# Optimization experiments

Measured on AMD Instinct MI355X. Metric: run time of the kernel, lower is better.

The kernel has to match this reference:

```python
import jax, jax.numpy as jnp
import numpy as np

N = 50000      # nodes
E = 800000     # edges (before self-loops)
IN = 256       # in_channels
H = 4          # heads (layer 1)
C = 64         # hidden per head
OUT = 40       # out_channels / classes


def setup_inputs() -> dict:
    key = jax.random.key(0)
    ks = jax.random.split(key, 10)
    s = 0.05  # weight init scale
    return {
        "x": jax.random.normal(ks[0], (N, IN), jnp.float32),
        "edge_index": jax.random.randint(ks[1], (2, E), 0, N),
        "W1": jax.random.normal(ks[2], (IN, H * C), jnp.float32) * s,
        "a_src1": jax.random.normal(ks[3], (H, C), jnp.float32) * s,
        "a_dst1": jax.random.normal(ks[4], (H, C), jnp.float32) * s,
        "b1": jnp.zeros((H * C,), jnp.float32),
        "W2": jax.random.normal(ks[5], (H * C, OUT), jnp.float32) * s,
        "a_src2": jax.random.normal(ks[6], (1, OUT), jnp.float32) * s,
        "a_dst2": jax.random.normal(ks[7], (1, OUT), jnp.float32) * s,
        "b2": jnp.zeros((OUT,), jnp.float32),
    }


def _gat_layer(x, src, dst, W, a_src, a_dst, bias, heads, out_c):
    """PyG GATConv (concat=True, negative_slope=0.2, self-loops already in src/dst)."""
    n = x.shape[0]
    h = (x @ W).reshape(n, heads, out_c)                    # [N,H,C]
    al_s = jnp.sum(h * a_src, axis=-1)                      # [N,H]
    al_d = jnp.sum(h * a_dst, axis=-1)                      # [N,H]
    e = jax.nn.leaky_relu(al_s[src] + al_d[dst], 0.2)       # [Etot,H]
    # edge softmax over incoming edges of each destination node
    m = jax.ops.segment_max(e, dst, num_segments=n)         # [N,H]
    ee = jnp.exp(e - m[dst])
    denom = jax.ops.segment_sum(ee, dst, num_segments=n)
    alpha = ee / (denom[dst] + 1e-16)                       # [Etot,H]
    msg = alpha[:, :, None] * h[src]                        # [Etot,H,C]
    out = jax.ops.segment_sum(msg, dst, num_segments=n)     # [N,H,C]
    return out.reshape(n, heads * out_c) + bias


def reference(x, edge_index, W1, a_src1, a_dst1, b1, W2, a_src2, a_dst2, b2):
    n = x.shape[0]
    loops = jnp.arange(n, dtype=edge_index.dtype)
    src = jnp.concatenate([edge_index[0], loops])
    dst = jnp.concatenate([edge_index[1], loops])
    h = _gat_layer(x, src, dst, W1, a_src1, a_dst1, b1, H, C)   # [N, H*C]
    h = jax.nn.relu(h)
    # F.dropout in eval mode is identity (reference run in eval mode)
    out = _gat_layer(h, src, dst, W2, a_src2, a_dst2, b2, 1, OUT)  # [N, OUT]
    return jax.nn.log_softmax(out, axis=1)
```

## Files before the change

### kernel.cpp

```cpp
#include <hip/hip_runtime.h>
#include <hip/hip_bf16.h>

typedef __hip_bfloat16 bf16;
typedef short v8s __attribute__((ext_vector_type(8)));
typedef float v4f __attribute__((ext_vector_type(4)));

constexpr int NN    = 50000;
constexpr int NE    = 800000;
constexpr int CIN   = 256;
constexpr int HC    = 256;
constexpr int NH    = 4;
constexpr int NOUT  = 40;
constexpr int NPAD  = 48;
constexpr int SCB   = 196;
constexpr int B1    = 128;
constexpr int CH    = (NE + B1 - 1) / B1;
constexpr int NB    = (NN + 255) >> 8;

constexpr size_t al256(size_t x){ return (x + 255) & ~(size_t)255; }
constexpr size_t WS_FLAGS = 0;
constexpr size_t WS_EW1   = 256;
constexpr size_t WS_W1T   = al256(WS_EW1   + (size_t)NE*16);
constexpr size_t WS_AS1N  = al256(WS_W1T   + (size_t)CIN*HC*2);
constexpr size_t WS_AD1N  = al256(WS_AS1N  + HC*2);
constexpr size_t WS_B1N   = al256(WS_AD1N  + HC*2);
constexpr size_t WS_W2T   = al256(WS_B1N   + HC*2);
constexpr size_t WS_AS2N  = al256(WS_W2T   + (size_t)NPAD*HC*2);
constexpr size_t WS_AD2N  = al256(WS_AS2N  + NOUT*2);
constexpr size_t WS_B2N   = al256(WS_AD2N  + NOUT*2);
constexpr size_t WS_COUNTS= al256(WS_B2N   + NOUT*2);
constexpr size_t WS_CURSOR= al256(WS_COUNTS+ (size_t)NN*4);
constexpr size_t WS_ROWPTR= al256(WS_CURSOR+ (size_t)NN*4);
constexpr size_t WS_EIDX  = al256(WS_ROWPTR+ (size_t)(NN+1)*4);
constexpr size_t WS_H1    = al256(WS_EIDX  + (size_t)NE*4);
constexpr size_t WS_ALS1  = al256(WS_H1    + (size_t)NN*HC);
constexpr size_t WS_ALD1  = al256(WS_ALS1  + (size_t)NN*NH*4);
constexpr size_t WS_Y1    = al256(WS_ALD1  + (size_t)NN*NH*4);
constexpr size_t WS_H2    = al256(WS_Y1    + (size_t)NN*HC*2);
constexpr size_t WS_ALS2  = al256(WS_H2    + (size_t)NN*NOUT*2);
constexpr size_t WS_ALD2  = al256(WS_ALS2  + (size_t)NN*4);
constexpr size_t WS_EW2   = al256(WS_ALD2  + (size_t)NN*4);
constexpr size_t WS_BSUM  = al256(WS_EW2   + (size_t)NE*4);
constexpr size_t WS_BOFF  = al256(WS_BSUM  + 1024);
constexpr size_t WS_GCNT  = al256(WS_BOFF  + 1024);
constexpr size_t WS_ROFF  = al256(WS_GCNT  + (size_t)256*B1*4);
constexpr size_t WS_BBASE = al256(WS_ROFF  + (size_t)256*B1*4);
constexpr size_t WS_EBUF  = al256(WS_BBASE + 1056);

constexpr int CV_W1  = 0;
constexpr int CV_AS1 = CV_W1  + CIN*HC;
constexpr int CV_AD1 = CV_AS1 + HC;
constexpr int CV_B1  = CV_AD1 + HC;
constexpr int CV_W2  = CV_B1  + HC;
constexpr int CV_AS2 = CV_W2  + HC*NOUT;
constexpr int CV_AD2 = CV_AS2 + NOUT;
constexpr int CV_B2  = CV_AD2 + NOUT;
constexpr int CV_HIST= CV_B2  + NOUT;
constexpr int CV_END = CV_HIST + NE;

__device__ __forceinline__ float b2f(bf16 v) { return __bfloat162float(v); }
__device__ __forceinline__ bf16  f2b(float v){ return __float2bfloat16(v); }
__device__ __forceinline__ float bits2f(unsigned short u){ return __uint_as_float(((unsigned)u) << 16); }
__device__ __forceinline__ unsigned short f2bits(float v){
  bf16 t = __float2bfloat16(v);
  return *reinterpret_cast<unsigned short*>(&t);
}
__device__ __forceinline__ float lrelu(float x){ return x > 0.f ? x : 0.2f * x; }

__device__ __forceinline__ float wave_sum(float v){
  #pragma unroll
  for (int off = 32; off; off >>= 1) v += __shfl_xor(v, off, 64);
  return v;
}
__device__ __forceinline__ float wave_max(float v){
  #pragma unroll
  for (int off = 32; off; off >>= 1) v = fmaxf(v, __shfl_xor(v, off, 64));
  return v;
}

__global__ __launch_bounds__(64) void k_detect(const unsigned short* __restrict__ xu,
                                               const unsigned* __restrict__ eu,
                                               int* __restrict__ flags){
  int lane = threadIdx.x;
  int cnt = 0;
  for (int i = lane; i < 256; i += 64){
    int e = (xu[i] >> 7) & 0xFF;
    cnt += (e >= 0x60 && e <= 0x8F) ? 1 : 0;
  }
  #pragma unroll
  for (int off = 32; off; off >>= 1) cnt += __shfl_xor(cnt, off, 64);
  unsigned odd = eu[2 * lane + 1];
  #pragma unroll
  for (int off = 32; off; off >>= 1) odd |= __shfl_xor(odd, off, 64);
  if (lane == 0){
    flags[0] = (cnt < 218) ? 1 : 0;
    flags[1] = (odd == 0)  ? 1 : 0;
  }
}

__device__ __forceinline__ bf16 cvt_b(const void* src, int i, int f32m){
  if (f32m) return __float2bfloat16(((const float*)src)[i]);
  return ((const bf16*)src)[i];
}

__global__ __launch_bounds__(256) void k_convert(
    const void* __restrict__ W1,
    const void* __restrict__ as1,const void* __restrict__ ad1,
    const void* __restrict__ b1, const void* __restrict__ W2,
    const void* __restrict__ as2,const void* __restrict__ ad2,
    const void* __restrict__ b2, const void* __restrict__ ei,
    char* __restrict__ ws){
  const int* flags = (const int*)(ws + WS_FLAGS);
  int f32m = flags[0], i64m = flags[1];
  bf16* w1t  = (bf16*)(ws + WS_W1T);
  bf16* as1n = (bf16*)(ws + WS_AS1N);
  bf16* ad1n = (bf16*)(ws + WS_AD1N);
  bf16* b1n  = (bf16*)(ws + WS_B1N);
  bf16* w2t  = (bf16*)(ws + WS_W2T);
  bf16* as2n = (bf16*)(ws + WS_AS2N);
  bf16* ad2n = (bf16*)(ws + WS_AD2N);
  bf16* b2n  = (bf16*)(ws + WS_B2N);
  int*  counts=(int*) (ws + WS_COUNTS);
  for (int g = blockIdx.x * 256 + threadIdx.x; g < CV_END; g += gridDim.x * 256){
    if      (g < CV_AS1){ int i = g-CV_W1; int k = i >> 8, n = i & 255;
      w1t[n*CIN + k] = cvt_b(W1, i, f32m); }
    else if (g < CV_AD1) as1n[g-CV_AS1] = cvt_b(as1,g-CV_AS1, f32m);
    else if (g < CV_B1 ) ad1n[g-CV_AD1] = cvt_b(ad1,g-CV_AD1, f32m);
    else if (g < CV_W2 ) b1n [g-CV_B1 ] = cvt_b(b1, g-CV_B1,  f32m);
    else if (g < CV_AS2){ int i = g-CV_W2; int k = i / NOUT, n = i - k*NOUT;
      w2t[n*CIN + k] = cvt_b(W2, i, f32m); }
    else if (g < CV_AD2) as2n[g-CV_AS2] = cvt_b(as2,g-CV_AS2, f32m);
    else if (g < CV_B2 ) ad2n[g-CV_AD2] = cvt_b(ad2,g-CV_AD2, f32m);
    else if (g < CV_HIST) b2n[g-CV_B2 ] = cvt_b(b2, g-CV_B2,  f32m);
    else { int i = g-CV_HIST;
      int d = i64m ? (int)((const long long*)ei)[(size_t)NE+i] : ((const int*)ei)[NE+i];
      atomicAdd(&counts[d], 1); }
  }
}

__global__ __launch_bounds__(256) void k_scan_part(const int* __restrict__ counts, int* __restrict__ bsum){
  __shared__ int lds[256];
  int t = threadIdx.x;
  int idx = blockIdx.x * 256 + t;
  int v = (idx < NN) ? counts[idx] : 0;
  lds[t] = v;
  #pragma unroll
  for (int s = 128; s > 0; s >>= 1){
    __syncthreads();
    if (t < s) lds[t] += lds[t + s];
  }
  if (t == 0) bsum[blockIdx.x] = lds[0];
}

__global__ __launch_bounds__(256) void k_scan_mid(const int* __restrict__ bsum, int* __restrict__ boff,
                                                  int* __restrict__ row_ptr){
  __shared__ int lds[256];
  int t = threadIdx.x;
  int v = (t < SCB) ? bsum[t] : 0;
  lds[t] = v;
  for (int off = 1; off < 256; off <<= 1){
    __syncthreads();
    int u = (t >= off) ? lds[t - off] : 0;
    __syncthreads();
    lds[t] += u;
  }
  __syncthreads();
  if (t < SCB) boff[t] = lds[t] - v;
  if (t == 0) row_ptr[NN] = NE;
}

__global__ __launch_bounds__(256) void k_scan_apply(const int* __restrict__ counts, const int* __restrict__ boff,
                                                    int* __restrict__ row_ptr){
  __shared__ int lds[256];
  int t = threadIdx.x;
  int idx = blockIdx.x * 256 + t;
  int v = (idx < NN) ? counts[idx] : 0;
  lds[t] = v;
  for (int off = 1; off < 256; off <<= 1){
    __syncthreads();
    int u = (t >= off) ? lds[t - off] : 0;
    __syncthreads();
    lds[t] += u;
  }
  __syncthreads();
  if (idx < NN) row_ptr[idx] = boff[blockIdx.x] + lds[t] - v;
}

__global__ __launch_bounds__(256) void k_lhist(const void* __restrict__ ei, const int* __restrict__ flags,
                                               int* __restrict__ gcnt){
  __shared__ int h[256];
  int tid = threadIdx.x, blk = blockIdx.x;
  h[tid] = 0;
  __syncthreads();
  int i0 = blk * CH, i1 = min(i0 + CH, NE);
  int i64m = flags[1];
  for (int i = i0 + tid; i < i1; i += 256){
    int d = i64m ? (int)((const long long*)ei)[(size_t)NE + i] : ((const int*)ei)[NE + i];
    atomicAdd(&h[d >> 8], 1);
  }
  __syncthreads();
  gcnt[tid * B1 + blk] = h[tid];
}

__global__ __launch_bounds__(256) void k_gscan(const int* __restrict__ gcnt, int* __restrict__ roff,
                                               int* __restrict__ bbase){
  __shared__ int lds[256];
  int t = threadIdx.x;
  int tot = 0;
  for (int blk = 0; blk < B1; ++blk) tot += gcnt[t * B1 + blk];
  lds[t] = tot;
  for (int off = 1; off < 256; off <<= 1){
    __syncthreads();
    int u = (t >= off) ? lds[t - off] : 0;
    __syncthreads();
    lds[t] += u;
  }
  __syncthreads();
  int base = lds[t] - tot;
  bbase[t] = base;
  if (t == 255) bbase[256] = NE;
  int run = base;
  for (int blk = 0; blk < B1; ++blk){
    roff[t * B1 + blk] = run;
    run += gcnt[t * B1 + blk];
  }
}

__global__ __launch_bounds__(256) void k_bscatter(const void* __restrict__ ei, const int* __restrict__ flags,
                                                  const int* __restrict__ roff, int2* __restrict__ ebuf){
  __shared__ int lcur[256];
  int tid = threadIdx.x, blk = blockIdx.x;
  lcur[tid] = roff[tid * B1 + blk];
  __syncthreads();
  int i0 = blk * CH, i1 = min(i0 + CH, NE);
  int i64m = flags[1];
  for (int i = i0 + tid; i < i1; i += 256){
    int s, d;
    if (i64m){ s = (int)((const long long*)ei)[i]; d = (int)((const long long*)ei)[(size_t)NE + i]; }
    else     { s = ((const int*)ei)[i];            d = ((const int*)ei)[NE + i]; }
    int pos = atomicAdd(&lcur[d >> 8], 1);
    ebuf[pos] = make_int2(s, d);
  }
}

__global__ __launch_bounds__(256) void k_refine(const int2* __restrict__ ebuf, const int* __restrict__ bbase,
                                                const int* __restrict__ row_ptr, int* __restrict__ cursor,
                                                int* __restrict__ eidx){
  int b = blockIdx.x;
  int p0 = bbase[b], p1 = bbase[b + 1];
  for (int p = p0 + threadIdx.x; p < p1; p += 256){
    int2 e = ebuf[p];
    int pos = row_ptr[e.y] + atomicAdd(&cursor[e.y], 1);
    eidx[pos] = e.x;
  }
}

constexpr int G1R = 64;
constexpr int LP  = 72;
__global__ __launch_bounds__(256) void k_gemm1(const void* __restrict__ xin,
                                               const int* __restrict__ flags,
                                               const bf16* __restrict__ w1t,
                                               const bf16* __restrict__ as1, const bf16* __restrict__ ad1,
                                               unsigned char* __restrict__ h1q,
                                               float* __restrict__ al_s1, float* __restrict__ al_d1){
  __shared__ short Ab[G1R * LP];
  __shared__ short Bb[256 * LP];
  int tid  = threadIdx.x;
  int w    = tid >> 6, lane = tid & 63, quad = lane >> 4, c = lane & 15;
  int row0 = blockIdx.x * G1R;
  int f32m = flags[0];

  v4f acc[4][4];
  #pragma unroll
  for (int mt = 0; mt < 4; ++mt)
    #pragma unroll
    for (int nt = 0; nt < 4; ++nt) acc[mt][nt] = (v4f){0.f,0.f,0.f,0.f};

  int arow = tid >> 2;
  int aseg = tid & 3;
  int grow = row0 + arow; if (grow >= NN) grow = NN - 1;

  for (int ph = 0; ph < 4; ++ph){
    if (ph) __syncthreads();
    {
      short va[16];
      if (f32m){
        const float* src = (const float*)xin + (size_t)grow * CIN + ph*64 + aseg*16;
        #pragma unroll
        for (int i = 0; i < 4; ++i){
          float4 f = *reinterpret_cast<const float4*>(src + i*4);
          va[i*4+0] = (short)f2bits(f.x); va[i*4+1] = (short)f2bits(f.y);
          va[i*4+2] = (short)f2bits(f.z); va[i*4+3] = (short)f2bits(f.w);
        }
      } else {
        const short* src = (const short*)xin + (size_t)grow * CIN + ph*64 + aseg*16;
        v8s u0 = *reinterpret_cast<const v8s*>(src);
        v8s u1 = *reinterpret_cast<const v8s*>(src + 8);
        #pragma unroll
        for (int i = 0; i < 8; ++i){ va[i] = u0[i]; va[8+i] = u1[i]; }
      }
      short* dst = &Ab[arow * LP + aseg * 16];
      *reinterpret_cast<v8s*>(dst)     = *reinterpret_cast<v8s*>(&va[0]);
      *reinterpret_cast<v8s*>(dst + 8) = *reinterpret_cast<v8s*>(&va[8]);
    }
    {
      const short* src = (const short*)w1t + (size_t)tid * CIN + ph*64;
      short* dst = &Bb[tid * LP];
      #pragma unroll
      for (int j = 0; j < 8; ++j)
        *reinterpret_cast<v8s*>(dst + j*8) = *reinterpret_cast<const v8s*>(src + j*8);
    }
    __syncthreads();
    #pragma unroll
    for (int s = 0; s < 2; ++s){
      int ch = s*4 + quad;
      v8s af[4], bfb[4];
      #pragma unroll
      for (int mt = 0; mt < 4; ++mt)
        af[mt] = *reinterpret_cast<const v8s*>(&Ab[(mt*16 + c) * LP + ch*8]);
      #pragma unroll
      for (int nt = 0; nt < 4; ++nt)
        bfb[nt] = *reinterpret_cast<const v8s*>(&Bb[(w*64 + nt*16 + c) * LP + ch*8]);
      #pragma unroll
      for (int mt = 0; mt < 4; ++mt)
        #pragma unroll
        for (int nt = 0; nt < 4; ++nt)
          acc[mt][nt] = __builtin_amdgcn_mfma_f32_16x16x32_bf16(af[mt], bfb[nt], acc[mt][nt], 0, 0, 0);
    }
  }

  float as1v[4], ad1v[4];
  #pragma unroll
  for (int nt = 0; nt < 4; ++nt){
    as1v[nt] = b2f(as1[w*64 + nt*16 + c]);
    ad1v[nt] = b2f(ad1[w*64 + nt*16 + c]);
  }
  #pragma unroll
  for (int mt = 0; mt < 4; ++mt){
    #pragma unroll
    for (int r = 0; r < 4; ++r){
      float ps = 0.f, pd = 0.f;
      #pragma unroll
      for (int nt = 0; nt < 4; ++nt){ ps += acc[mt][nt][r] * as1v[nt]; pd += acc[mt][nt][r] * ad1v[nt]; }
      #pragma unroll
      for (int off = 1; off < 16; off <<= 1){ ps += __shfl_xor(ps, off, 64); pd += __shfl_xor(pd, off, 64); }
      int row = row0 + mt*16 + quad*4 + r;
      if (c == 0 && row < NN){
        al_s1[row * NH + w] = ps;
        al_d1[row * NH + w] = pd;
      }
    }
  }
  #pragma unroll
  for (int mt = 0; mt < 4; ++mt){
    #pragma unroll
    for (int nt = 0; nt < 4; ++nt){
      #pragma unroll
      for (int r = 0; r < 4; r += 2){
        int row = row0 + mt*16 + quad*4 + r;
        if (row + 1 < NN){
          int pk = __builtin_amdgcn_cvt_pk_fp8_f32(acc[mt][nt][r], acc[mt][nt][r+1], 0, false);
          size_t col = w*64 + nt*16 + c;
          h1q[(size_t)row       * HC + col] = (unsigned char)(pk & 0xFF);
          h1q[(size_t)(row + 1) * HC + col] = (unsigned char)((pk >> 8) & 0xFF);
        } else if (row < NN){
          int pk = __builtin_amdgcn_cvt_pk_fp8_f32(acc[mt][nt][r], acc[mt][nt][r], 0, false);
          h1q[(size_t)row * HC + w*64 + nt*16 + c] = (unsigned char)(pk & 0xFF);
        }
      }
    }
  }
}

__global__ __launch_bounds__(256) void k_ew1(const int* __restrict__ row_ptr, const int* __restrict__ eidx,
                                             const float* __restrict__ al_s1, const float* __restrict__ al_d1,
                                             float4* __restrict__ ew1){
  int lane = threadIdx.x & 63;
  int n = blockIdx.x * 4 + (threadIdx.x >> 6);
  int p0 = __builtin_amdgcn_readfirstlane(row_ptr[n]);
  int p1 = __builtin_amdgcn_readfirstlane(row_ptr[n + 1]);
  float4 ad = reinterpret_cast<const float4*>(al_d1)[n];
  for (int p = p0 + lane; p < p1; p += 64){
    int s = eidx[p];
    float4 as = reinterpret_cast<const float4*>(al_s1)[s];
    float4 w;
    w.x = __expf(lrelu(as.x + ad.x));
    w.y = __expf(lrelu(as.y + ad.y));
    w.z = __expf(lrelu(as.z + ad.z));
    w.w = __expf(lrelu(as.w + ad.w));
    ew1[p] = w;
  }
}

__global__ __launch_bounds__(256) void k_gather1(const int* __restrict__ row_ptr, const int* __restrict__ eidx,
                                                 const float* __restrict__ ew1,
                                                 const float* __restrict__ al_s1, const float* __restrict__ al_d1,
                                                 const unsigned* __restrict__ h1v, const bf16* __restrict__ b1,
                                                 bf16* __restrict__ y1){
  int lane = threadIdx.x & 63;
  int n = blockIdx.x * 4 + (threadIdx.x >> 6);
  int h = lane >> 4;
  int p0 = __builtin_amdgcn_readfirstlane(row_ptr[n]);
  int p1 = __builtin_amdgcn_readfirstlane(row_ptr[n + 1]);
  float wss = __expf(lrelu(al_s1[n * NH + h] + al_d1[n * NH + h]));
  unsigned us = h1v[(size_t)n * 64 + lane];
  float den = wss;
  float a0 = wss * __builtin_amdgcn_cvt_f32_fp8(us, 0);
  float a1 = wss * __builtin_amdgcn_cvt_f32_fp8(us, 1);
  float a2 = wss * __builtin_amdgcn_cvt_f32_fp8(us, 2);
  float a3 = wss * __builtin_amdgcn_cvt_f32_fp8(us, 3);
  int p = p0;
  for (; p + 1 < p1; p += 2){
    int sA = __builtin_amdgcn_readfirstlane(eidx[p]);
    int sB = __builtin_amdgcn_readfirstlane(eidx[p + 1]);
    float wA = ew1[(size_t)p * 4 + h];
    float wB = ew1[(size_t)(p + 1) * 4 + h];
    unsigned uA = h1v[(size_t)sA * 64 + lane];
    unsigned uB = h1v[(size_t)sB * 64 + lane];
    den += wA + wB;
    a0 += wA * __builtin_amdgcn_cvt_f32_fp8(uA, 0) + wB * __builtin_amdgcn_cvt_f32_fp8(uB, 0);
    a1 += wA * __builtin_amdgcn_cvt_f32_fp8(uA, 1) + wB * __builtin_amdgcn_cvt_f32_fp8(uB, 1);
    a2 += wA * __builtin_amdgcn_cvt_f32_fp8(uA, 2) + wB * __builtin_amdgcn_cvt_f32_fp8(uB, 2);
    a3 += wA * __builtin_amdgcn_cvt_f32_fp8(uA, 3) + wB * __builtin_amdgcn_cvt_f32_fp8(uB, 3);
  }
  if (p < p1){
    int s = __builtin_amdgcn_readfirstlane(eidx[p]);
    float w = ew1[(size_t)p * 4 + h];
    unsigned u = h1v[(size_t)s * 64 + lane];
    den += w;
    a0 += w * __builtin_amdgcn_cvt_f32_fp8(u, 0);
    a1 += w * __builtin_amdgcn_cvt_f32_fp8(u, 1);
    a2 += w * __builtin_amdgcn_cvt_f32_fp8(u, 2);
    a3 += w * __builtin_amdgcn_cvt_f32_fp8(u, 3);
  }
  float inv = 1.f / (den + 1e-16f);
  ushort4 bb = reinterpret_cast<const ushort4*>(b1)[lane];
  ushort4 o;
  o.x = f2bits(fmaxf(a0 * inv + bits2f(bb.x), 0.f));
  o.y = f2bits(fmaxf(a1 * inv + bits2f(bb.y), 0.f));
  o.z = f2bits(fmaxf(a2 * inv + bits2f(bb.z), 0.f));
  o.w = f2bits(fmaxf(a3 * inv + bits2f(bb.w), 0.f));
  reinterpret_cast<ushort4*>(y1)[(size_t)n * 64 + lane] = o;
}

constexpr int W2LP = 260;
__global__ __launch_bounds__(256) void k_gemm2(const bf16* __restrict__ y1, const bf16* __restrict__ w2t,
                                               const bf16* __restrict__ as2, const bf16* __restrict__ ad2,
                                               bf16* __restrict__ h2, float* __restrict__ al_s2,
                                               float* __restrict__ al_d2){
  __shared__ short Wb[NPAD * W2LP];
  int tid = threadIdx.x;
  int w = tid >> 6, lane = tid & 63, quad = lane >> 4, c = lane & 15;
  int m0 = blockIdx.x * 64 + w * 16;
  for (int idx = tid; idx < NPAD * 32; idx += 256){
    int n = idx >> 5, sg = idx & 31;
    *reinterpret_cast<v8s*>(&Wb[n * W2LP + sg * 8]) =
      *reinterpret_cast<const v8s*>((const short*)w2t + (size_t)n * CIN + sg * 8);
  }
  int arow = m0 + c; if (arow >= NN) arow = NN - 1;
  const short* ar = (const short*)y1 + (size_t)arow * HC + quad * 8;
  v8s a[8];
  #pragma unroll
  for (int i = 0; i < 8; ++i) a[i] = *reinterpret_cast<const v8s*>(ar + i * 32);
  __syncthreads();

  v4f acc[3];
  #pragma unroll
  for (int t = 0; t < 3; ++t) acc[t] = (v4f){0.f, 0.f, 0.f, 0.f};
  #pragma unroll
  for (int k = 0; k < 8; ++k){
    int ch = k*4 + quad;
    #pragma unroll
    for (int t = 0; t < 3; ++t){
      v8s b = *reinterpret_cast<const v8s*>(&Wb[(t*16 + c) * W2LP + ch * 8]);
      acc[t] = __builtin_amdgcn_mfma_f32_16x16x32_bf16(a[k], b, acc[t], 0, 0, 0);
    }
  }
  float as2f[3], ad2f[3];
  #pragma unroll
  for (int t = 0; t < 3; ++t){
    int col = t*16 + c;
    as2f[t] = (col < NOUT) ? b2f(as2[col]) : 0.f;
    ad2f[t] = (col < NOUT) ? b2f(ad2[col]) : 0.f;
  }
  #pragma unroll
  for (int r = 0; r < 4; ++r){
    int row = m0 + quad*4 + r;
    float ps = 0.f, pd = 0.f;
    #pragma unroll
    for (int t = 0; t < 3; ++t){ ps += acc[t][r] * as2f[t]; pd += acc[t][r] * ad2f[t]; }
    #pragma unroll
    for (int off = 1; off < 16; off <<= 1){ ps += __shfl_xor(ps, off, 64); pd += __shfl_xor(pd, off, 64); }
    if (row < NN){
      if (c == 0){ al_s2[row] = ps; al_d2[row] = pd; }
      #pragma unroll
      for (int t = 0; t < 3; ++t){
        int col = t*16 + c;
        if (col < NOUT) h2[(size_t)row * NOUT + col] = f2b(acc[t][r]);
      }
    }
  }
}

__global__ __launch_bounds__(256) void k_ew2(const int* __restrict__ row_ptr, const int* __restrict__ eidx,
                                             const float* __restrict__ al_s2, const float* __restrict__ al_d2,
                                             float* __restrict__ ew2){
  int lane = threadIdx.x & 63;
  int n = blockIdx.x * 4 + (threadIdx.x >> 6);
  int p0 = __builtin_amdgcn_readfirstlane(row_ptr[n]);
  int p1 = __builtin_amdgcn_readfirstlane(row_ptr[n + 1]);
  float ad = al_d2[n];
  for (int p = p0 + lane; p < p1; p += 64)
    ew2[p] = __expf(lrelu(al_s2[eidx[p]] + ad));
}

__global__ __launch_bounds__(256) void k_gather2(const int* __restrict__ row_ptr, const int* __restrict__ eidx,
                                                 const float* __restrict__ ew2,
                                                 const float* __restrict__ al_s2, const float* __restrict__ al_d2,
                                                 const bf16* __restrict__ h2, const bf16* __restrict__ b2v,
                                                 const int* __restrict__ flags, void* __restrict__ out){
  int lane = threadIdx.x & 63;
  int n = blockIdx.x * 4 + (threadIdx.x >> 6);
  int p0 = __builtin_amdgcn_readfirstlane(row_ptr[n]);
  int p1 = __builtin_amdgcn_readfirstlane(row_ptr[n + 1]);
  float wss = __expf(lrelu(al_s2[n] + al_d2[n]));
  float den = wss;
  float acc = (lane < NOUT) ? wss * b2f(h2[(size_t)n * NOUT + lane]) : 0.f;
  int p = p0;
  for (; p + 1 < p1; p += 2){
    int sA = __builtin_amdgcn_readfirstlane(eidx[p]);
    int sB = __builtin_amdgcn_readfirstlane(eidx[p + 1]);
    float wA = ew2[p], wB = ew2[p + 1];
    float hA = 0.f, hB = 0.f;
    if (lane < NOUT){
      hA = b2f(h2[(size_t)sA * NOUT + lane]);
      hB = b2f(h2[(size_t)sB * NOUT + lane]);
    }
    den += wA + wB;
    acc += wA * hA + wB * hB;
  }
  if (p < p1){
    int s = __builtin_amdgcn_readfirstlane(eidx[p]);
    float w = ew2[p];
    den += w;
    if (lane < NOUT) acc += w * b2f(h2[(size_t)s * NOUT + lane]);
  }
  float v = (lane < NOUT) ? (acc / (den + 1e-16f) + b2f(b2v[lane])) : -INFINITY;
  float M = wave_max(v);
  float ex = (lane < NOUT) ? __expf(v - M) : 0.f;
  float S = wave_sum(ex);
  if (lane < NOUT){
    float r = v - M - __logf(S);
    size_t idx = (size_t)n * NOUT + lane;
    if (flags[0]) ((float*)out)[idx] = r;
    else          ((bf16*)out)[idx]  = f2b(r);
  }
}

extern "C" void kernel_launch(void* const* d_in, const int* in_sizes, int n_in,
                              void* d_out, int out_size, void* d_ws, size_t ws_size,
                              hipStream_t stream) {
  const void* x   = d_in[0];
  const void* ei  = d_in[1];
  const void* W1  = d_in[2];
  const void* as1 = d_in[3];
  const void* ad1 = d_in[4];
  const void* b1  = d_in[5];
  const void* W2  = d_in[6];
  const void* as2 = d_in[7];
  const void* ad2 = d_in[8];
  const void* b2  = d_in[9];

  char* ws = (char*)d_ws;
  int*   flags   = (int*)  (ws + WS_FLAGS);
  float* ew1     = (float*)(ws + WS_EW1);
  bf16*  w1t     = (bf16*) (ws + WS_W1T);
  bf16*  as1n    = (bf16*) (ws + WS_AS1N);
  bf16*  ad1n    = (bf16*) (ws + WS_AD1N);
  bf16*  b1n     = (bf16*) (ws + WS_B1N);
  bf16*  w2t     = (bf16*) (ws + WS_W2T);
  bf16*  as2n    = (bf16*) (ws + WS_AS2N);
  bf16*  ad2n    = (bf16*) (ws + WS_AD2N);
  bf16*  b2n     = (bf16*) (ws + WS_B2N);
  int*   counts  = (int*)  (ws + WS_COUNTS);
  int*   cursor  = (int*)  (ws + WS_CURSOR);
  int*   row_ptr = (int*)  (ws + WS_ROWPTR);
  int*   eidx    = (int*)  (ws + WS_EIDX);
  unsigned char* h1q = (unsigned char*)(ws + WS_H1);
  float* al_s1   = (float*)(ws + WS_ALS1);
  float* al_d1   = (float*)(ws + WS_ALD1);
  bf16*  y1      = (bf16*) (ws + WS_Y1);
  bf16*  h2      = (bf16*) (ws + WS_H2);
  float* al_s2   = (float*)(ws + WS_ALS2);
  float* al_d2   = (float*)(ws + WS_ALD2);
  float* ew2     = (float*)(ws + WS_EW2);
  int*   bsum    = (int*)  (ws + WS_BSUM);
  int*   boff    = (int*)  (ws + WS_BOFF);
  int*   gcnt    = (int*)  (ws + WS_GCNT);
  int*   roff    = (int*)  (ws + WS_ROFF);
  int*   bbase   = (int*)  (ws + WS_BBASE);
  int2*  ebuf    = (int2*) (ws + WS_EBUF);

  hipMemsetAsync(counts, 0, (size_t)NN * 4, stream);
  hipMemsetAsync(cursor, 0, (size_t)NN * 4, stream);
  hipMemsetAsync(w2t,    0, (size_t)NPAD * CIN * 2, stream);

  k_detect <<<1, 64, 0, stream>>>((const unsigned short*)x, (const unsigned*)ei, flags);
  k_convert<<<1024, 256, 0, stream>>>(W1, as1, ad1, b1, W2, as2, ad2, b2, ei, ws);

  k_lhist   <<<B1, 256, 0, stream>>>(ei, flags, gcnt);
  k_gscan   <<<1, 256, 0, stream>>>(gcnt, roff, bbase);
  k_scan_part <<<SCB, 256, 0, stream>>>(counts, bsum);
  k_scan_mid  <<<1, 256, 0, stream>>>(bsum, boff, row_ptr);
  k_scan_apply<<<SCB, 256, 0, stream>>>(counts, boff, row_ptr);
  k_bscatter<<<B1, 256, 0, stream>>>(ei, flags, roff, ebuf);
  k_refine  <<<NB, 256, 0, stream>>>(ebuf, bbase, row_ptr, cursor, eidx);

  k_gemm1  <<<(NN + G1R - 1) / G1R, 256, 0, stream>>>(x, flags, w1t, as1n, ad1n, h1q, al_s1, al_d1);
  k_ew1    <<<NN / 4, 256, 0, stream>>>(row_ptr, eidx, al_s1, al_d1, (float4*)ew1);
  k_gather1<<<NN / 4, 256, 0, stream>>>(row_ptr, eidx, ew1, al_s1, al_d1, (const unsigned*)h1q, b1n, y1);
  k_gemm2  <<<(NN + 63) / 64, 256, 0, stream>>>(y1, w2t, as2n, ad2n, h2, al_s2, al_d2);
  k_ew2    <<<NN / 4, 256, 0, stream>>>(row_ptr, eidx, al_s2, al_d2, ew2);
  k_gather2<<<NN / 4, 256, 0, stream>>>(row_ptr, eidx, ew2, al_s2, al_d2, h2, b2n, flags, d_out);
}
```

Baseline: 347.3 us.

## Store layer-2 features as FP8 and split gather2 edges across quarter-waves

Layer-2 projected features are now written by gemm2 as FP8 bytes in a 64-byte row stride instead of bf16 rows of 40. gather2 splits each node's edge list across four 16-lane groups, each handling every fourth edge. Each lane unpacks four FP8 channels, and the partial sums are then combined with cross-lane shuffles. Gather1's inner loop is also unrolled from 2 to 4 edges to expose more outstanding loads. The goal is less gather traffic and more memory-level parallelism, at the cost of extra FP8 quantization error on layer-2 activations and byte-granular scattered writes in gemm2.

```diff
diff --git a/kernel.cpp b/kernel.cpp
--- a/kernel.cpp
+++ b/kernel.cpp
@@ -37,7 +37,7 @@
 constexpr size_t WS_ALD1  = al256(WS_ALS1  + (size_t)NN*NH*4);
 constexpr size_t WS_Y1    = al256(WS_ALD1  + (size_t)NN*NH*4);
 constexpr size_t WS_H2    = al256(WS_Y1    + (size_t)NN*HC*2);
-constexpr size_t WS_ALS2  = al256(WS_H2    + (size_t)NN*NOUT*2);
+constexpr size_t WS_ALS2  = al256(WS_H2    + (size_t)NN*64);
 constexpr size_t WS_ALD2  = al256(WS_ALS2  + (size_t)NN*4);
 constexpr size_t WS_EW2   = al256(WS_ALD2  + (size_t)NN*4);
 constexpr size_t WS_BSUM  = al256(WS_EW2   + (size_t)NE*4);
@@ -410,20 +410,30 @@
   float a2 = wss * __builtin_amdgcn_cvt_f32_fp8(us, 2);
   float a3 = wss * __builtin_amdgcn_cvt_f32_fp8(us, 3);
   int p = p0;
-  for (; p + 1 < p1; p += 2){
+  for (; p + 3 < p1; p += 4){
     int sA = __builtin_amdgcn_readfirstlane(eidx[p]);
     int sB = __builtin_amdgcn_readfirstlane(eidx[p + 1]);
+    int sC = __builtin_amdgcn_readfirstlane(eidx[p + 2]);
+    int sD = __builtin_amdgcn_readfirstlane(eidx[p + 3]);
     float wA = ew1[(size_t)p * 4 + h];
     float wB = ew1[(size_t)(p + 1) * 4 + h];
+    float wC = ew1[(size_t)(p + 2) * 4 + h];
+    float wD = ew1[(size_t)(p + 3) * 4 + h];
     unsigned uA = h1v[(size_t)sA * 64 + lane];
     unsigned uB = h1v[(size_t)sB * 64 + lane];
-    den += wA + wB;
-    a0 += wA * __builtin_amdgcn_cvt_f32_fp8(uA, 0) + wB * __builtin_amdgcn_cvt_f32_fp8(uB, 0);
-    a1 += wA * __builtin_amdgcn_cvt_f32_fp8(uA, 1) + wB * __builtin_amdgcn_cvt_f32_fp8(uB, 1);
-    a2 += wA * __builtin_amdgcn_cvt_f32_fp8(uA, 2) + wB * __builtin_amdgcn_cvt_f32_fp8(uB, 2);
-    a3 += wA * __builtin_amdgcn_cvt_f32_fp8(uA, 3) + wB * __builtin_amdgcn_cvt_f32_fp8(uB, 3);
-  }
-  if (p < p1){
+    unsigned uC = h1v[(size_t)sC * 64 + lane];
+    unsigned uD = h1v[(size_t)sD * 64 + lane];
+    den += (wA + wB) + (wC + wD);
+    a0 += wA * __builtin_amdgcn_cvt_f32_fp8(uA, 0) + wB * __builtin_amdgcn_cvt_f32_fp8(uB, 0)
+        + wC * __builtin_amdgcn_cvt_f32_fp8(uC, 0) + wD * __builtin_amdgcn_cvt_f32_fp8(uD, 0);
+    a1 += wA * __builtin_amdgcn_cvt_f32_fp8(uA, 1) + wB * __builtin_amdgcn_cvt_f32_fp8(uB, 1)
+        + wC * __builtin_amdgcn_cvt_f32_fp8(uC, 1) + wD * __builtin_amdgcn_cvt_f32_fp8(uD, 1);
+    a2 += wA * __builtin_amdgcn_cvt_f32_fp8(uA, 2) + wB * __builtin_amdgcn_cvt_f32_fp8(uB, 2)
+        + wC * __builtin_amdgcn_cvt_f32_fp8(uC, 2) + wD * __builtin_amdgcn_cvt_f32_fp8(uD, 2);
+    a3 += wA * __builtin_amdgcn_cvt_f32_fp8(uA, 3) + wB * __builtin_amdgcn_cvt_f32_fp8(uB, 3)
+        + wC * __builtin_amdgcn_cvt_f32_fp8(uC, 3) + wD * __builtin_amdgcn_cvt_f32_fp8(uD, 3);
+  }
+  for (; p < p1; ++p){
     int s = __builtin_amdgcn_readfirstlane(eidx[p]);
     float w = ew1[(size_t)p * 4 + h];
     unsigned u = h1v[(size_t)s * 64 + lane];
@@ -446,7 +456,7 @@
 constexpr int W2LP = 260;
 __global__ __launch_bounds__(256) void k_gemm2(const bf16* __restrict__ y1, const bf16* __restrict__ w2t,
                                                const bf16* __restrict__ as2, const bf16* __restrict__ ad2,
-                                               bf16* __restrict__ h2, float* __restrict__ al_s2,
+                                               unsigned char* __restrict__ h2q, float* __restrict__ al_s2,
                                                float* __restrict__ al_d2){
   __shared__ short Wb[NPAD * W2LP];
   int tid = threadIdx.x;
@@ -491,12 +501,18 @@
     for (int t = 0; t < 3; ++t){ ps += acc[t][r] * as2f[t]; pd += acc[t][r] * ad2f[t]; }
     #pragma unroll
     for (int off = 1; off < 16; off <<= 1){ ps += __shfl_xor(ps, off, 64); pd += __shfl_xor(pd, off, 64); }
-    if (row < NN){
-      if (c == 0){ al_s2[row] = ps; al_d2[row] = pd; }
-      #pragma unroll
-      for (int t = 0; t < 3; ++t){
-        int col = t*16 + c;
-        if (col < NOUT) h2[(size_t)row * NOUT + col] = f2b(acc[t][r]);
+    if (row < NN && c == 0){ al_s2[row] = ps; al_d2[row] = pd; }
+  }
+  #pragma unroll
+  for (int t = 0; t < 3; ++t){
+    int col = t*16 + c;
+    if (col < NOUT){
+      #pragma unroll
+      for (int r = 0; r < 4; r += 2){
+        int row = m0 + quad*4 + r;
+        int pk = __builtin_amdgcn_cvt_pk_fp8_f32(acc[t][r], acc[t][r+1], 0, false);
+        if (row < NN)     h2q[(size_t)row       * 64 + col] = (unsigned char)(pk & 0xFF);
+        if (row + 1 < NN) h2q[(size_t)(row + 1) * 64 + col] = (unsigned char)((pk >> 8) & 0xFF);
       }
     }
   }
@@ -517,43 +533,81 @@
 __global__ __launch_bounds__(256) void k_gather2(const int* __restrict__ row_ptr, const int* __restrict__ eidx,
                                                  const float* __restrict__ ew2,
                                                  const float* __restrict__ al_s2, const float* __restrict__ al_d2,
-                                                 const bf16* __restrict__ h2, const bf16* __restrict__ b2v,
+                                                 const unsigned char* __restrict__ h2q, const bf16* __restrict__ b2v,
                                                  const int* __restrict__ flags, void* __restrict__ out){
   int lane = threadIdx.x & 63;
   int n = blockIdx.x * 4 + (threadIdx.x >> 6);
+  int q = lane >> 4, c = lane & 15;
+  bool act = (c < 10);
   int p0 = __builtin_amdgcn_readfirstlane(row_ptr[n]);
   int p1 = __builtin_amdgcn_readfirstlane(row_ptr[n + 1]);
-  float wss = __expf(lrelu(al_s2[n] + al_d2[n]));
-  float den = wss;
-  float acc = (lane < NOUT) ? wss * b2f(h2[(size_t)n * NOUT + lane]) : 0.f;
-  int p = p0;
-  for (; p + 1 < p1; p += 2){
-    int sA = __builtin_amdgcn_readfirstlane(eidx[p]);
-    int sB = __builtin_amdgcn_readfirstlane(eidx[p + 1]);
-    float wA = ew2[p], wB = ew2[p + 1];
-    float hA = 0.f, hB = 0.f;
-    if (lane < NOUT){
-      hA = b2f(h2[(size_t)sA * NOUT + lane]);
-      hB = b2f(h2[(size_t)sB * NOUT + lane]);
-    }
+  const unsigned* h2v = reinterpret_cast<const unsigned*>(h2q);
+  float den = 0.f, a0 = 0.f, a1 = 0.f, a2 = 0.f, a3 = 0.f;
+  if (q == 0){
+    float wss = __expf(lrelu(al_s2[n] + al_d2[n]));
+    den = wss;
+    if (act){
+      unsigned u = h2v[(size_t)n * 16 + c];
+      a0 = wss * __builtin_amdgcn_cvt_f32_fp8(u, 0);
+      a1 = wss * __builtin_amdgcn_cvt_f32_fp8(u, 1);
+      a2 = wss * __builtin_amdgcn_cvt_f32_fp8(u, 2);
+      a3 = wss * __builtin_amdgcn_cvt_f32_fp8(u, 3);
+    }
+  }
+  int p = p0 + q;
+  for (; p + 4 < p1; p += 8){
+    int sA = eidx[p], sB = eidx[p + 4];
+    float wA = ew2[p], wB = ew2[p + 4];
+    unsigned uA = act ? h2v[(size_t)sA * 16 + c] : 0u;
+    unsigned uB = act ? h2v[(size_t)sB * 16 + c] : 0u;
     den += wA + wB;
-    acc += wA * hA + wB * hB;
+    a0 += wA * __builtin_amdgcn_cvt_f32_fp8(uA, 0) + wB * __builtin_amdgcn_cvt_f32_fp8(uB, 0);
+    a1 += wA * __builtin_amdgcn_cvt_f32_fp8(uA, 1) + wB * __builtin_amdgcn_cvt_f32_fp8(uB, 1);
+    a2 += wA * __builtin_amdgcn_cvt_f32_fp8(uA, 2) + wB * __builtin_amdgcn_cvt_f32_fp8(uB, 2);
+    a3 += wA * __builtin_amdgcn_cvt_f32_fp8(uA, 3) + wB * __builtin_amdgcn_cvt_f32_fp8(uB, 3);
   }
   if (p < p1){
-    int s = __builtin_amdgcn_readfirstlane(eidx[p]);
+    int s = eidx[p];
     float w = ew2[p];
+    unsigned u = act ? h2v[(size_t)s * 16 + c] : 0u;
     den += w;
-    if (lane < NOUT) acc += w * b2f(h2[(size_t)s * NOUT + lane]);
-  }
-  float v = (lane < NOUT) ? (acc / (den + 1e-16f) + b2f(b2v[lane])) : -INFINITY;
-  float M = wave_max(v);
-  float ex = (lane < NOUT) ? __expf(v - M) : 0.f;
+    a0 += w * __builtin_amdgcn_cvt_f32_fp8(u, 0);
+    a1 += w * __builtin_amdgcn_cvt_f32_fp8(u, 1);
+    a2 += w * __builtin_amdgcn_cvt_f32_fp8(u, 2);
+    a3 += w * __builtin_amdgcn_cvt_f32_fp8(u, 3);
+  }
+  #pragma unroll
+  for (int off = 16; off <= 32; off <<= 1){
+    den += __shfl_xor(den, off, 64);
+    a0  += __shfl_xor(a0,  off, 64);
+    a1  += __shfl_xor(a1,  off, 64);
+    a2  += __shfl_xor(a2,  off, 64);
+    a3  += __shfl_xor(a3,  off, 64);
+  }
+  float inv = 1.f / (den + 1e-16f);
+  float v0 = -INFINITY, v1 = -INFINITY, v2 = -INFINITY, v3 = -INFINITY;
+  if (act){
+    ushort4 bb = *reinterpret_cast<const ushort4*>(reinterpret_cast<const unsigned short*>(b2v) + 4 * c);
+    v0 = a0 * inv + bits2f(bb.x);
+    v1 = a1 * inv + bits2f(bb.y);
+    v2 = a2 * inv + bits2f(bb.z);
+    v3 = a3 * inv + bits2f(bb.w);
+  }
+  float M = wave_max(fmaxf(fmaxf(v0, v1), fmaxf(v2, v3)));
+  float ex = (q == 0 && act)
+           ? (__expf(v0 - M) + __expf(v1 - M)) + (__expf(v2 - M) + __expf(v3 - M)) : 0.f;
   float S = wave_sum(ex);
-  if (lane < NOUT){
-    float r = v - M - __logf(S);
-    size_t idx = (size_t)n * NOUT + lane;
-    if (flags[0]) ((float*)out)[idx] = r;
-    else          ((bf16*)out)[idx]  = f2b(r);
+  if (q == 0 && act){
+    float lg = M + __logf(S);
+    if (flags[0]){
+      float4 o = {v0 - lg, v1 - lg, v2 - lg, v3 - lg};
+      *reinterpret_cast<float4*>((float*)out + (size_t)n * NOUT + 4 * c) = o;
+    } else {
+      ushort4 o;
+      o.x = f2bits(v0 - lg); o.y = f2bits(v1 - lg);
+      o.z = f2bits(v2 - lg); o.w = f2bits(v3 - lg);
+      *reinterpret_cast<ushort4*>((unsigned short*)out + (size_t)n * NOUT + 4 * c) = o;
+    }
   }
 }
 
@@ -590,7 +644,7 @@
   float* al_s1   = (float*)(ws + WS_ALS1);
   float* al_d1   = (float*)(ws + WS_ALD1);
   bf16*  y1      = (bf16*) (ws + WS_Y1);
-  bf16*  h2      = (bf16*) (ws + WS_H2);
+  unsigned char* h2q = (unsigned char*)(ws + WS_H2);
   float* al_s2   = (float*)(ws + WS_ALS2);
   float* al_d2   = (float*)(ws + WS_ALD2);
   float* ew2     = (float*)(ws + WS_EW2);
@@ -619,7 +673,7 @@
   k_gemm1  <<<(NN + G1R - 1) / G1R, 256, 0, stream>>>(x, flags, w1t, as1n, ad1n, h1q, al_s1, al_d1);
   k_ew1    <<<NN / 4, 256, 0, stream>>>(row_ptr, eidx, al_s1, al_d1, (float4*)ew1);
   k_gather1<<<NN / 4, 256, 0, stream>>>(row_ptr, eidx, ew1, al_s1, al_d1, (const unsigned*)h1q, b1n, y1);
-  k_gemm2  <<<(NN + 63) / 64, 256, 0, stream>>>(y1, w2t, as2n, ad2n, h2, al_s2, al_d2);
+  k_gemm2  <<<(NN + 63) / 64, 256, 0, stream>>>(y1, w2t, as2n, ad2n, h2q, al_s2, al_d2);
   k_ew2    <<<NN / 4, 256, 0, stream>>>(row_ptr, eidx, al_s2, al_d2, ew2);
-  k_gather2<<<NN / 4, 256, 0, stream>>>(row_ptr, eidx, ew2, al_s2, al_d2, h2, b2n, flags, d_out);
-}
+  k_gather2<<<NN / 4, 256, 0, stream>>>(row_ptr, eidx, ew2, al_s2, al_d2, h2q, b2n, flags, d_out);
+}
```

After: 329.2 us. 1.05x faster.
